# Kernel tuning notes

Measured on AMD Instinct MI355X. Metric: run time of the kernel, lower is better.

The kernel has to match this reference:

```python
import jax, jax.numpy as jnp
import numpy as np

N = 50000
E = 800000
IN_DIM = 256
HID = 64
HEADS = 4
OUT_DIM = 40
NEG_SLOPE = 0.2


def _gatv2_conv(x, src, dst, Wl, bl, Wr, br, att, bias, concat):
    """PyG GATv2Conv (share_weights=False, eval mode, no attn dropout).
    src -> message source nodes, dst -> target nodes (softmax over dst)."""
    H, C = att.shape
    n = x.shape[0]
    xl = (x @ Wl + bl).reshape(n, H, C)  # source/message transform (lin_l)
    xr = (x @ Wr + br).reshape(n, H, C)  # target transform (lin_r)
    # per-edge logits: [E, H]
    s = xl[src] + xr[dst]                                  # [E,H,C]
    e = jnp.einsum('ehc,hc->eh', jax.nn.leaky_relu(s, NEG_SLOPE), att)
    # segment softmax over incoming edges of each target node
    m = jax.ops.segment_max(e, dst, num_segments=n)        # [N,H]
    m = jnp.where(jnp.isfinite(m), m, 0.0)                 # empty segments
    ex = jnp.exp(e - m[dst])
    denom = jax.ops.segment_sum(ex, dst, num_segments=n)   # [N,H]
    alpha = ex / (denom[dst] + 1e-16)                      # [E,H]
    out = jax.ops.segment_sum(alpha[:, :, None] * xl[src], dst, num_segments=n)
    if concat:
        out = out.reshape(n, H * C)
    else:
        out = out.mean(axis=1)
    return out + bias


def setup_inputs() -> dict:
    key = jax.random.key(0)
    ks = jax.random.split(key, 12)
    sc = 0.05
    return {
        'x': jax.random.normal(ks[0], (N, IN_DIM), jnp.float32),
        'src': jax.random.randint(ks[1], (E,), 0, N, jnp.int32),
        'dst': jax.random.randint(ks[2], (E,), 0, N, jnp.int32),
        'Wl1': jax.random.normal(ks[3], (IN_DIM, HEADS * HID), jnp.float32) * sc,
        'bl1': jnp.zeros((HEADS * HID,), jnp.float32),
        'Wr1': jax.random.normal(ks[4], (IN_DIM, HEADS * HID), jnp.float32) * sc,
        'br1': jnp.zeros((HEADS * HID,), jnp.float32),
        'att1': jax.random.normal(ks[5], (HEADS, HID), jnp.float32) * sc,
        'bias1': jnp.zeros((HEADS * HID,), jnp.float32),
        'Wl2': jax.random.normal(ks[6], (HEADS * HID, HEADS * HID), jnp.float32) * sc,
        'bl2': jnp.zeros((HEADS * HID,), jnp.float32),
        'Wr2': jax.random.normal(ks[7], (HEADS * HID, HEADS * HID), jnp.float32) * sc,
        'br2': jnp.zeros((HEADS * HID,), jnp.float32),
        'att2': jax.random.normal(ks[8], (HEADS, HID), jnp.float32) * sc,
        'bias2': jnp.zeros((HID,), jnp.float32),
        'Wc': jax.random.normal(ks[9], (HID, OUT_DIM), jnp.float32) * sc,
        'bc': jnp.zeros((OUT_DIM,), jnp.float32),
    }


def reference(x, src, dst, Wl1, bl1, Wr1, br1, att1, bias1,
              Wl2, bl2, Wr2, br2, att2, bias2, Wc, bc):
    h = _gatv2_conv(x, src, dst, Wl1, bl1, Wr1, br1, att1, bias1, concat=True)
    h = jax.nn.relu(h)  # dropout p applied only in training; eval -> identity
    h = _gatv2_conv(h, src, dst, Wl2, bl2, Wr2, br2, att2, bias2, concat=False)
    h = jax.nn.relu(h)
    return h @ Wc + bc  # [N, OUT_DIM]
```

## Files before the change

### kernel.cpp

```cpp
#include <hip/hip_runtime.h>
#include <hip/hip_bf16.h>
#include <math.h>


#define IN_DIM 256
#define HIDHC 256
#define HID 64
#define OUT_DIM 40

using half8  = __attribute__((ext_vector_type(8))) _Float16;
using half4  = __attribute__((ext_vector_type(4))) _Float16;
using half2v = __attribute__((ext_vector_type(2))) _Float16;
using f32x4  = __attribute__((ext_vector_type(4))) float;

__device__ __forceinline__ void gload16(const void* g, void* l) {
    __builtin_amdgcn_global_load_lds(
        (const __attribute__((address_space(1))) void*)g,
        (__attribute__((address_space(3))) void*)l, 16, 0, 0);
}


__global__ void edge_hist(const int* __restrict__ dst, int* __restrict__ deg, int E) {
    int i = blockIdx.x * blockDim.x + threadIdx.x;
    if (i < E) atomicAdd(&deg[dst[i]], 1);
}

__global__ void deg_block_reduce(const int* __restrict__ deg, int* __restrict__ bsum, int n) {
    int i = blockIdx.x * 256 + threadIdx.x;
    int v = (i < n) ? deg[i] : 0;
    #pragma unroll
    for (int off = 32; off; off >>= 1) v += __shfl_xor(v, off, 64);
    __shared__ int ws[4];
    int lane = threadIdx.x & 63, wid = threadIdx.x >> 6;
    if (lane == 0) ws[wid] = v;
    __syncthreads();
    if (threadIdx.x == 0) bsum[blockIdx.x] = ws[0] + ws[1] + ws[2] + ws[3];
}

__global__ void scan_bsums(const int* __restrict__ bsum, int* __restrict__ bpre, int nb) {
    __shared__ int s[256];
    int tid = threadIdx.x;
    int orig = (tid < nb) ? bsum[tid] : 0;
    s[tid] = orig;
    __syncthreads();
    #pragma unroll
    for (int off = 1; off < 256; off <<= 1) {
        int t = (tid >= off) ? s[tid - off] : 0;
        __syncthreads();
        s[tid] += t;
        __syncthreads();
    }
    if (tid < nb) bpre[tid] = s[tid] - orig;
}

__global__ void deg_scan_apply(const int* __restrict__ deg, const int* __restrict__ bpre,
                               int* __restrict__ offsets, int* __restrict__ cursor, int n) {
    int i = blockIdx.x * 256 + threadIdx.x;
    int lane = threadIdx.x & 63, wid = threadIdx.x >> 6;
    int v = (i < n) ? deg[i] : 0;
    int inc = v;
    #pragma unroll
    for (int off = 1; off < 64; off <<= 1) {
        int t = __shfl_up(inc, off, 64);
        if (lane >= off) inc += t;
    }
    __shared__ int ws[4];
    if (lane == 63) ws[wid] = inc;
    __syncthreads();
    int add = bpre[blockIdx.x];
    for (int w = 0; w < wid; ++w) add += ws[w];
    int incl = inc + add;
    if (i < n) { offsets[i + 1] = incl; cursor[i] = incl - v; }
    if (i == 0) offsets[0] = 0;
}

__global__ void edge_scatter(const int* __restrict__ src, const int* __restrict__ dst,
                             int* __restrict__ cursor, int* __restrict__ csr_src, int E) {
    int i = blockIdx.x * blockDim.x + threadIdx.x;
    if (i < E) {
        int p = atomicAdd(&cursor[dst[i]], 1);
        csr_src[p] = src[i];
    }
}


__global__ void cvt_f16(const float* __restrict__ in, _Float16* __restrict__ out, int n4) {
    int i = blockIdx.x * blockDim.x + threadIdx.x;
    if (i >= n4) return;
    float4 v = ((const float4*)in)[i];
    half4 h = { (_Float16)v.x, (_Float16)v.y, (_Float16)v.z, (_Float16)v.w };
    ((half4*)out)[i] = h;
}

__global__ void prep_weights(const float* __restrict__ W0, const float* __restrict__ W1,
                             const float* __restrict__ W2, const float* __restrict__ W3,
                             _Float16* __restrict__ T) {
    const float* Wsel = (blockIdx.y == 0) ? W0 : (blockIdx.y == 1) ? W1
                      : (blockIdx.y == 2) ? W2 : W3;
    int k = blockIdx.x, nn = threadIdx.x;
    float v = Wsel[k * 256 + nn];
    T[(size_t)blockIdx.y * 65536 + (size_t)nn * 256 + k] = (_Float16)v;
}


__global__ __launch_bounds__(256) void gemm2_mfma(
    const _Float16* __restrict__ A,
    const _Float16* __restrict__ W0, const float* __restrict__ b0, _Float16* __restrict__ C0,
    const _Float16* __restrict__ W1, const float* __restrict__ b1, _Float16* __restrict__ C1,
    int M)
{
    __shared__ __align__(16) _Float16 sA[2][4096], sB[2][4096];

    const _Float16* W   = blockIdx.z ? W1 : W0;
    const float*    bias= blockIdx.z ? b1 : b0;
    _Float16*       C   = blockIdx.z ? C1 : C0;

    int tid = threadIdx.x;
    int bm = blockIdx.x * 128;
    int bn = blockIdx.y * 128;

    int lane = tid & 63, w = tid >> 6;
    int r = lane & 15, q = lane >> 4;
    int m0 = (w >> 1) * 64, n0 = (w & 1) * 64;

    int arow[2], brow[2], kgo[2], lds[2];
    #pragma unroll
    for (int i = 0; i < 2; ++i) {
        int g = tid + 256 * i;
        kgo[i] = (g >> 7) * 8;
        int row = g & 127;
        arow[i] = min(bm + row, M - 1);
        brow[i] = bn + row;
        lds[i] = g * 8;
    }

    f32x4 acc[4][4];
    #pragma unroll
    for (int i = 0; i < 4; ++i)
        #pragma unroll
        for (int j = 0; j < 4; ++j) acc[i][j] = (f32x4)0.f;

    #pragma unroll
    for (int i = 0; i < 2; ++i) {
        gload16(A + (size_t)arow[i] * 256 + kgo[i], &sA[0][lds[i]]);
        gload16(W + (size_t)brow[i] * 256 + kgo[i], &sB[0][lds[i]]);
    }
    __builtin_amdgcn_s_waitcnt(0);
    __syncthreads();

    #pragma unroll 1
    for (int kt = 0; kt < 8; ++kt) {
        int buf = kt & 1;
        if (kt < 7) {
            int k0 = (kt + 1) * 32;
            #pragma unroll
            for (int i = 0; i < 2; ++i) {
                gload16(A + (size_t)arow[i] * 256 + k0 + kgo[i], &sA[buf ^ 1][lds[i]]);
                gload16(W + (size_t)brow[i] * 256 + k0 + kgo[i], &sB[buf ^ 1][lds[i]]);
            }
        }
        half8 a[4], b[4];
        #pragma unroll
        for (int i = 0; i < 4; ++i) {
            a[i] = *(const half8*)(&sA[buf][(q * 128 + m0 + i * 16 + r) * 8]);
            b[i] = *(const half8*)(&sB[buf][(q * 128 + n0 + i * 16 + r) * 8]);
        }
        #pragma unroll
        for (int i = 0; i < 4; ++i)
            #pragma unroll
            for (int j = 0; j < 4; ++j)
                acc[i][j] = __builtin_amdgcn_mfma_f32_16x16x32_f16(a[i], b[j], acc[i][j], 0, 0, 0);
        __builtin_amdgcn_s_waitcnt(0);
        __syncthreads();
    }

    float bv[4];
    #pragma unroll
    for (int j = 0; j < 4; ++j) bv[j] = bias[bn + n0 + j * 16 + r];
    #pragma unroll
    for (int i = 0; i < 4; ++i) {
        #pragma unroll
        for (int reg = 0; reg < 4; ++reg) {
            int row = bm + m0 + i * 16 + q * 4 + reg;
            if (row < M) {
                #pragma unroll
                for (int j = 0; j < 4; ++j)
                    C[(size_t)row * 256 + bn + n0 + j * 16 + r] =
                        (_Float16)(acc[i][j][reg] + bv[j]);
            }
        }
    }
}


__global__ __launch_bounds__(256) void gat_node(
    const _Float16* __restrict__ xl, const _Float16* __restrict__ xr,
    const float* __restrict__ att, const float* __restrict__ bias,
    const int* __restrict__ offsets, const int* __restrict__ csr_src,
    void* __restrict__ out0, int n, int mode)
{
    int wid = threadIdx.x >> 6;
    int node = (blockIdx.x << 2) + wid;
    if (node >= n) return;
    int lane = threadIdx.x & 63;
    int H = lane >> 5;
    int p = lane & 31;

    const half2v c02 = { (_Float16)0.2f, (_Float16)0.2f };

    half8 xrh = *(const half8*)(xr + (size_t)node * HIDHC + p * 8);
    half2v xr01 = __builtin_shufflevector(xrh, xrh, 0, 1);
    half2v xr23 = __builtin_shufflevector(xrh, xrh, 2, 3);
    half2v xr45 = __builtin_shufflevector(xrh, xrh, 4, 5);
    half2v xr67 = __builtin_shufflevector(xrh, xrh, 6, 7);

    float4 af0 = *(const float4*)(att + p * 8);
    float4 af1 = *(const float4*)(att + p * 8 + 4);
    half2v at01 = { (_Float16)af0.x, (_Float16)af0.y };
    half2v at23 = { (_Float16)af0.z, (_Float16)af0.w };
    half2v at45 = { (_Float16)af1.x, (_Float16)af1.y };
    half2v at67 = { (_Float16)af1.z, (_Float16)af1.w };

    float acc[8];
    #pragma unroll
    for (int k = 0; k < 8; ++k) acc[k] = 0.f;
    float d = 0.f;

    int j0 = __builtin_amdgcn_readfirstlane(offsets[node]);
    int j1 = __builtin_amdgcn_readfirstlane(offsets[node + 1]);
    int deg = j1 - j0;

    int fast = min(deg, 64);
    int npf = fast >> 1;
    int idxv = 0;
    if (lane < fast) idxv = csr_src[j0 + lane];

    half8 h0, h1;
    if (npf > 0) {
        int s = __shfl(idxv, H, 64);
        h0 = *(const half8*)(xl + (size_t)s * HIDHC + p * 8);
    }
    if (npf > 1) {
        int s = __shfl(idxv, 2 + H, 64);
        h1 = *(const half8*)(xl + (size_t)s * HIDHC + p * 8);
    }
    for (int t = 0; t < npf; ++t) {
        half8 h = h0;
        h0 = h1;
        if (t + 2 < npf) {
            int s = __shfl(idxv, (t + 2) * 2 + H, 64);
            h1 = *(const half8*)(xl + (size_t)s * HIDHC + p * 8);
        }
        half2v h01 = __builtin_shufflevector(h, h, 0, 1);
        half2v h23 = __builtin_shufflevector(h, h, 2, 3);
        half2v h45 = __builtin_shufflevector(h, h, 4, 5);
        half2v h67 = __builtin_shufflevector(h, h, 6, 7);
        half2v s01 = h01 + xr01, s23 = h23 + xr23, s45 = h45 + xr45, s67 = h67 + xr67;
        half2v l01 = __builtin_elementwise_max(s01, s01 * c02);
        half2v l23 = __builtin_elementwise_max(s23, s23 * c02);
        half2v l45 = __builtin_elementwise_max(s45, s45 * c02);
        half2v l67 = __builtin_elementwise_max(s67, s67 * c02);
        float e = __builtin_amdgcn_fdot2(l01, at01, 0.f, false);
        e = __builtin_amdgcn_fdot2(l23, at23, e, false);
        e = __builtin_amdgcn_fdot2(l45, at45, e, false);
        e = __builtin_amdgcn_fdot2(l67, at67, e, false);
        e += __shfl_xor(e, 1);
        e += __shfl_xor(e, 2);
        e += __shfl_xor(e, 4);
        float pw = __expf(e);
        d += pw;
        #pragma unroll
        for (int k = 0; k < 8; ++k) acc[k] = fmaf(pw, (float)h[k], acc[k]);
    }

    int j = j0 + (npf << 1);
    for (; j + 2 <= j1; j += 2) {
        int s0 = __builtin_amdgcn_readfirstlane(csr_src[j]);
        int s1 = __builtin_amdgcn_readfirstlane(csr_src[j + 1]);
        int s = H ? s1 : s0;
        half8 h = *(const half8*)(xl + (size_t)s * HIDHC + p * 8);
        half2v h01 = __builtin_shufflevector(h, h, 0, 1);
        half2v h23 = __builtin_shufflevector(h, h, 2, 3);
        half2v h45 = __builtin_shufflevector(h, h, 4, 5);
        half2v h67 = __builtin_shufflevector(h, h, 6, 7);
        half2v s01 = h01 + xr01, s23 = h23 + xr23, s45 = h45 + xr45, s67 = h67 + xr67;
        half2v l01 = __builtin_elementwise_max(s01, s01 * c02);
        half2v l23 = __builtin_elementwise_max(s23, s23 * c02);
        half2v l45 = __builtin_elementwise_max(s45, s45 * c02);
        half2v l67 = __builtin_elementwise_max(s67, s67 * c02);
        float e = __builtin_amdgcn_fdot2(l01, at01, 0.f, false);
        e = __builtin_amdgcn_fdot2(l23, at23, e, false);
        e = __builtin_amdgcn_fdot2(l45, at45, e, false);
        e = __builtin_amdgcn_fdot2(l67, at67, e, false);
        e += __shfl_xor(e, 1);
        e += __shfl_xor(e, 2);
        e += __shfl_xor(e, 4);
        float pw = __expf(e);
        d += pw;
        #pragma unroll
        for (int k = 0; k < 8; ++k) acc[k] = fmaf(pw, (float)h[k], acc[k]);
    }
    if (j < j1) {
        int s0 = __builtin_amdgcn_readfirstlane(csr_src[j]);
        half8 h = *(const half8*)(xl + (size_t)s0 * HIDHC + p * 8);
        half2v h01 = __builtin_shufflevector(h, h, 0, 1);
        half2v h23 = __builtin_shufflevector(h, h, 2, 3);
        half2v h45 = __builtin_shufflevector(h, h, 4, 5);
        half2v h67 = __builtin_shufflevector(h, h, 6, 7);
        half2v s01 = h01 + xr01, s23 = h23 + xr23, s45 = h45 + xr45, s67 = h67 + xr67;
        half2v l01 = __builtin_elementwise_max(s01, s01 * c02);
        half2v l23 = __builtin_elementwise_max(s23, s23 * c02);
        half2v l45 = __builtin_elementwise_max(s45, s45 * c02);
        half2v l67 = __builtin_elementwise_max(s67, s67 * c02);
        float e = __builtin_amdgcn_fdot2(l01, at01, 0.f, false);
        e = __builtin_amdgcn_fdot2(l23, at23, e, false);
        e = __builtin_amdgcn_fdot2(l45, at45, e, false);
        e = __builtin_amdgcn_fdot2(l67, at67, e, false);
        e += __shfl_xor(e, 1);
        e += __shfl_xor(e, 2);
        e += __shfl_xor(e, 4);
        float pw = (H == 0) ? __expf(e) : 0.f;
        d += pw;
        #pragma unroll
        for (int k = 0; k < 8; ++k) acc[k] = fmaf(pw, (float)h[k], acc[k]);
    }

    d += __shfl_xor(d, 32);
    #pragma unroll
    for (int k = 0; k < 8; ++k) acc[k] += __shfl_xor(acc[k], 32);

    float inv = 1.f / (d + 1e-16f);
    float o[8];
    #pragma unroll
    for (int k = 0; k < 8; ++k) o[k] = acc[k] * inv;

    if (mode == 0) {
        if (H == 0) {
            float4 b0 = *(const float4*)(bias + p * 8);
            float4 b1 = *(const float4*)(bias + p * 8 + 4);
            float bb[8] = { b0.x, b0.y, b0.z, b0.w, b1.x, b1.y, b1.z, b1.w };
            half8 hh;
            #pragma unroll
            for (int k = 0; k < 8; ++k) hh[k] = (_Float16)fmaxf(o[k] + bb[k], 0.f);
            *(half8*)((_Float16*)out0 + (size_t)node * HIDHC + p * 8) = hh;
        }
    } else {
        #pragma unroll
        for (int k = 0; k < 8; ++k) {
            o[k] += __shfl_xor(o[k], 8);
            o[k] += __shfl_xor(o[k], 16);
        }
        if (lane < 8) {
            float4 b0 = *(const float4*)(bias + p * 8);
            float4 b1 = *(const float4*)(bias + p * 8 + 4);
            float bb[8] = { b0.x, b0.y, b0.z, b0.w, b1.x, b1.y, b1.z, b1.w };
            float4 o0, o1;
            o0.x = fmaxf(o[0] * 0.25f + bb[0], 0.f);
            o0.y = fmaxf(o[1] * 0.25f + bb[1], 0.f);
            o0.z = fmaxf(o[2] * 0.25f + bb[2], 0.f);
            o0.w = fmaxf(o[3] * 0.25f + bb[3], 0.f);
            o1.x = fmaxf(o[4] * 0.25f + bb[4], 0.f);
            o1.y = fmaxf(o[5] * 0.25f + bb[5], 0.f);
            o1.z = fmaxf(o[6] * 0.25f + bb[6], 0.f);
            o1.w = fmaxf(o[7] * 0.25f + bb[7], 0.f);
            float* dst = (float*)out0 + (size_t)node * HID + p * 8;
            *(float4*)dst = o0;
            *(float4*)(dst + 4) = o1;
        }
    }
}


__global__ __launch_bounds__(256) void final_linear(
    const float* __restrict__ h2, const float* __restrict__ Wc,
    const float* __restrict__ bc, float* __restrict__ out, int n)
{
    __shared__ float Ws[HID * OUT_DIM];
    __shared__ float bs[OUT_DIM];
    __shared__ float hs[64][HID + 1];

    for (int i = threadIdx.x; i < HID * OUT_DIM; i += 256) Ws[i] = Wc[i];
    if (threadIdx.x < OUT_DIM) bs[threadIdx.x] = bc[threadIdx.x];

    int n0 = blockIdx.x * 64;
    for (int i = threadIdx.x; i < 64 * HID; i += 256) {
        int r = i >> 6, c = i & 63;
        int node = n0 + r;
        hs[r][c] = (node < n) ? h2[(size_t)node * HID + c] : 0.f;
    }
    __syncthreads();

    for (int idx = threadIdx.x; idx < 64 * OUT_DIM; idx += 256) {
        int r = idx / OUT_DIM, o = idx % OUT_DIM;
        int node = n0 + r;
        if (node < n) {
            float s = bs[o];
            #pragma unroll
            for (int c = 0; c < HID; ++c) s = fmaf(hs[r][c], Ws[c * OUT_DIM + o], s);
            out[(size_t)node * OUT_DIM + o] = s;
        }
    }
}


extern "C" void kernel_launch(void* const* d_in, const int* in_sizes, int n_in,
                              void* d_out, int out_size, void* d_ws, size_t ws_size,
                              hipStream_t stream) {
    const int N = in_sizes[0] / IN_DIM;
    const int E = in_sizes[1];

    const float* x    = (const float*)d_in[0];
    const int*   src  = (const int*)d_in[1];
    const int*   dst  = (const int*)d_in[2];
    const float* Wl1  = (const float*)d_in[3];
    const float* bl1  = (const float*)d_in[4];
    const float* Wr1  = (const float*)d_in[5];
    const float* br1  = (const float*)d_in[6];
    const float* att1 = (const float*)d_in[7];
    const float* bias1= (const float*)d_in[8];
    const float* Wl2  = (const float*)d_in[9];
    const float* bl2  = (const float*)d_in[10];
    const float* Wr2  = (const float*)d_in[11];
    const float* br2  = (const float*)d_in[12];
    const float* att2 = (const float*)d_in[13];
    const float* bias2= (const float*)d_in[14];
    const float* Wc   = (const float*)d_in[15];
    const float* bc   = (const float*)d_in[16];

    char* ws = (char*)d_ws;
    size_t off = 0;
    _Float16* xlh = (_Float16*)(ws + off); off += (size_t)N * HIDHC * 2;
    _Float16* xrh = (_Float16*)(ws + off); off += (size_t)N * HIDHC * 2;
    _Float16* Af  = (_Float16*)(ws + off); off += (size_t)N * HIDHC * 2;
    float*    h2  = (float*)(ws + off);    off += (size_t)N * HID * 4;
    _Float16* Wt  = (_Float16*)(ws + off); off += (size_t)4 * 65536 * 2;
    int* deg     = (int*)(ws + off); off += (size_t)N * 4;
    int* offsets = (int*)(ws + off); off += (size_t)(N + 1) * 4;
    int* cursor  = (int*)(ws + off); off += (size_t)N * 4;
    int* csr     = (int*)(ws + off); off += (size_t)E * 4;
    int* bsum    = (int*)(ws + off); off += 256 * 4;
    int* bpre    = (int*)(ws + off); off += 256 * 4;

    const int NB = (N + 255) / 256;

    hipMemsetAsync(deg, 0, (size_t)N * 4, stream);
    edge_hist<<<(E + 255) / 256, 256, 0, stream>>>(dst, deg, E);
    deg_block_reduce<<<NB, 256, 0, stream>>>(deg, bsum, N);
    scan_bsums<<<1, 256, 0, stream>>>(bsum, bpre, NB);
    deg_scan_apply<<<NB, 256, 0, stream>>>(deg, bpre, offsets, cursor, N);
    edge_scatter<<<(E + 255) / 256, 256, 0, stream>>>(src, dst, cursor, csr, E);
    prep_weights<<<dim3(256, 4), 256, 0, stream>>>(Wl1, Wr1, Wl2, Wr2, Wt);
    cvt_f16<<<(N * HIDHC / 4 + 255) / 256, 256, 0, stream>>>(x, Af, N * HIDHC / 4);

    const int KW = 65536;
    dim3 gg((N + 127) / 128, 2, 2);
    gemm2_mfma<<<gg, 256, 0, stream>>>(Af,
        Wt + 0 * KW, bl1, xlh,
        Wt + 1 * KW, br1, xrh, N);
    gat_node<<<(N + 3) / 4, 256, 0, stream>>>(xlh, xrh, att1, bias1, offsets, csr,
                                              (void*)Af, N, 0);
    gemm2_mfma<<<gg, 256, 0, stream>>>(Af,
        Wt + 2 * KW, bl2, xlh,
        Wt + 3 * KW, br2, xrh, N);
    gat_node<<<(N + 3) / 4, 256, 0, stream>>>(xlh, xrh, att2, bias2, offsets, csr,
                                              (void*)h2, N, 1);
    final_linear<<<(N + 63) / 64, 256, 0, stream>>>(h2, Wc, bc, (float*)d_out, N);
}
```

Measured before the change: 464.6 us.

## Share A tile across both weight GEMMs and deepen gather prefetch

The two lin_l/lin_r GEMMs now run as one 512-thread block: the A tile is loaded into LDS once and shared by two groups of four waves, each group multiplying by its own weight matrix. Before, a separate block was launched per weight matrix via blockIdx.z, so every A tile was fetched twice. Separately, the GAT node kernel's neighbour-feature gather prefetch is deepened from two to four outstanding loads to hide more memory latency. The cost is larger LDS per block and more live registers, which may reduce occupancy.

```diff
diff --git a/kernel.cpp b/kernel.cpp
--- a/kernel.cpp
+++ b/kernel.cpp
@@ -103,36 +103,30 @@
 }
 
 
-__global__ __launch_bounds__(256) void gemm2_mfma(
+__global__ __launch_bounds__(512) void gemm_dual(
     const _Float16* __restrict__ A,
     const _Float16* __restrict__ W0, const float* __restrict__ b0, _Float16* __restrict__ C0,
     const _Float16* __restrict__ W1, const float* __restrict__ b1, _Float16* __restrict__ C1,
     int M)
 {
-    __shared__ __align__(16) _Float16 sA[2][4096], sB[2][4096];
-
-    const _Float16* W   = blockIdx.z ? W1 : W0;
-    const float*    bias= blockIdx.z ? b1 : b0;
-    _Float16*       C   = blockIdx.z ? C1 : C0;
+    __shared__ __align__(16) _Float16 sA[2][4096];
+    __shared__ __align__(16) _Float16 sW[2][2][4096];
 
     int tid = threadIdx.x;
     int bm = blockIdx.x * 128;
     int bn = blockIdx.y * 128;
 
     int lane = tid & 63, w = tid >> 6;
+    int z  = w >> 2, wq = w & 3;
     int r = lane & 15, q = lane >> 4;
-    int m0 = (w >> 1) * 64, n0 = (w & 1) * 64;
-
-    int arow[2], brow[2], kgo[2], lds[2];
-    #pragma unroll
-    for (int i = 0; i < 2; ++i) {
-        int g = tid + 256 * i;
-        kgo[i] = (g >> 7) * 8;
-        int row = g & 127;
-        arow[i] = min(bm + row, M - 1);
-        brow[i] = bn + row;
-        lds[i] = g * 8;
-    }
+    int m0 = (wq >> 1) * 64, n0 = (wq & 1) * 64;
+
+    int g = tid;
+    int kgo = (g >> 7) * 8;
+    int row = g & 127;
+    int arow = min(bm + row, M - 1);
+    int brow = bn + row;
+    int ldso = g * 8;
 
     f32x4 acc[4][4];
     #pragma unroll
@@ -140,11 +134,9 @@
         #pragma unroll
         for (int j = 0; j < 4; ++j) acc[i][j] = (f32x4)0.f;
 
-    #pragma unroll
-    for (int i = 0; i < 2; ++i) {
-        gload16(A + (size_t)arow[i] * 256 + kgo[i], &sA[0][lds[i]]);
-        gload16(W + (size_t)brow[i] * 256 + kgo[i], &sB[0][lds[i]]);
-    }
+    gload16(A  + (size_t)arow * 256 + kgo, &sA[0][ldso]);
+    gload16(W0 + (size_t)brow * 256 + kgo, &sW[0][0][ldso]);
+    gload16(W1 + (size_t)brow * 256 + kgo, &sW[0][1][ldso]);
     __builtin_amdgcn_s_waitcnt(0);
     __syncthreads();
 
@@ -153,17 +145,15 @@
         int buf = kt & 1;
         if (kt < 7) {
             int k0 = (kt + 1) * 32;
-            #pragma unroll
-            for (int i = 0; i < 2; ++i) {
-                gload16(A + (size_t)arow[i] * 256 + k0 + kgo[i], &sA[buf ^ 1][lds[i]]);
-                gload16(W + (size_t)brow[i] * 256 + k0 + kgo[i], &sB[buf ^ 1][lds[i]]);
-            }
+            gload16(A  + (size_t)arow * 256 + k0 + kgo, &sA[buf ^ 1][ldso]);
+            gload16(W0 + (size_t)brow * 256 + k0 + kgo, &sW[buf ^ 1][0][ldso]);
+            gload16(W1 + (size_t)brow * 256 + k0 + kgo, &sW[buf ^ 1][1][ldso]);
         }
         half8 a[4], b[4];
         #pragma unroll
         for (int i = 0; i < 4; ++i) {
             a[i] = *(const half8*)(&sA[buf][(q * 128 + m0 + i * 16 + r) * 8]);
-            b[i] = *(const half8*)(&sB[buf][(q * 128 + n0 + i * 16 + r) * 8]);
+            b[i] = *(const half8*)(&sW[buf][z][(q * 128 + n0 + i * 16 + r) * 8]);
         }
         #pragma unroll
         for (int i = 0; i < 4; ++i)
@@ -174,6 +164,9 @@
         __syncthreads();
     }
 
+    const float* bias = z ? b1 : b0;
+    _Float16*    C    = z ? C1 : C0;
+
     float bv[4];
     #pragma unroll
     for (int j = 0; j < 4; ++j) bv[j] = bias[bn + n0 + j * 16 + r];
@@ -181,11 +174,11 @@
     for (int i = 0; i < 4; ++i) {
         #pragma unroll
         for (int reg = 0; reg < 4; ++reg) {
-            int row = bm + m0 + i * 16 + q * 4 + reg;
-            if (row < M) {
+            int orow = bm + m0 + i * 16 + q * 4 + reg;
+            if (orow < M) {
                 #pragma unroll
                 for (int j = 0; j < 4; ++j)
-                    C[(size_t)row * 256 + bn + n0 + j * 16 + r] =
+                    C[(size_t)orow * 256 + bn + n0 + j * 16 + r] =
                         (_Float16)(acc[i][j][reg] + bv[j]);
             }
         }
@@ -235,21 +228,17 @@
     int idxv = 0;
     if (lane < fast) idxv = csr_src[j0 + lane];
 
-    half8 h0, h1;
-    if (npf > 0) {
-        int s = __shfl(idxv, H, 64);
-        h0 = *(const half8*)(xl + (size_t)s * HIDHC + p * 8);
-    }
-    if (npf > 1) {
-        int s = __shfl(idxv, 2 + H, 64);
-        h1 = *(const half8*)(xl + (size_t)s * HIDHC + p * 8);
-    }
+    half8 hb0, hb1, hb2, hb3;
+    if (npf > 0) { int s = __shfl(idxv, 0 + H, 64); hb0 = *(const half8*)(xl + (size_t)s * HIDHC + p * 8); }
+    if (npf > 1) { int s = __shfl(idxv, 2 + H, 64); hb1 = *(const half8*)(xl + (size_t)s * HIDHC + p * 8); }
+    if (npf > 2) { int s = __shfl(idxv, 4 + H, 64); hb2 = *(const half8*)(xl + (size_t)s * HIDHC + p * 8); }
+    if (npf > 3) { int s = __shfl(idxv, 6 + H, 64); hb3 = *(const half8*)(xl + (size_t)s * HIDHC + p * 8); }
     for (int t = 0; t < npf; ++t) {
-        half8 h = h0;
-        h0 = h1;
-        if (t + 2 < npf) {
-            int s = __shfl(idxv, (t + 2) * 2 + H, 64);
-            h1 = *(const half8*)(xl + (size_t)s * HIDHC + p * 8);
+        half8 h = hb0;
+        hb0 = hb1; hb1 = hb2; hb2 = hb3;
+        if (t + 4 < npf) {
+            int s = __shfl(idxv, (t + 4) * 2 + H, 64);
+            hb3 = *(const half8*)(xl + (size_t)s * HIDHC + p * 8);
         }
         half2v h01 = __builtin_shufflevector(h, h, 0, 1);
         half2v h23 = __builtin_shufflevector(h, h, 2, 3);
@@ -453,13 +442,13 @@
     cvt_f16<<<(N * HIDHC / 4 + 255) / 256, 256, 0, stream>>>(x, Af, N * HIDHC / 4);
 
     const int KW = 65536;
-    dim3 gg((N + 127) / 128, 2, 2);
-    gemm2_mfma<<<gg, 256, 0, stream>>>(Af,
+    dim3 gg((N + 127) / 128, 2);
+    gemm_dual<<<gg, 512, 0, stream>>>(Af,
         Wt + 0 * KW, bl1, xlh,
         Wt + 1 * KW, br1, xrh, N);
     gat_node<<<(N + 3) / 4, 256, 0, stream>>>(xlh, xrh, att1, bias1, offsets, csr,
                                               (void*)Af, N, 0);
-    gemm2_mfma<<<gg, 256, 0, stream>>>(Af,
+    gemm_dual<<<gg, 512, 0, stream>>>(Af,
         Wt + 2 * KW, bl2, xlh,
         Wt + 3 * KW, br2, xrh, N);
     gat_node<<<(N + 3) / 4, 256, 0, stream>>>(xlh, xrh, att2, bias2, offsets, csr,
```

After: 445.2 us. 4.2% less time.
